# Optimization experiments

Measured on AMD Instinct MI355X. Metric: run time of the kernel, lower is better.

Reference implementation:

```python
import jax, jax.numpy as jnp
import numpy as np

EPS = float(np.finfo(np.float32).eps)
QMIN, QMAX = -128, 127


def setup_inputs() -> dict:
    key = jax.random.key(0)
    k_x, k_w, k_ws, k_b = jax.random.split(key, 4)
    M, K, N = 32768, 1024, 1024
    x = jax.random.normal(k_x, (M, K), dtype=jnp.float32)
    # per-channel symmetrically quantized, transposed weight: [K, N], values in [-128, 127]
    w_int8_t = jax.random.randint(k_w, (K, N), QMIN, QMAX + 1, dtype=jnp.int32).astype(jnp.int8)
    # per-out-channel scales (positive, float; torch uses float64, we use float32)
    w_scales = (jax.random.uniform(k_ws, (N,), dtype=jnp.float32) * 0.02 + 1e-4)
    # preprocessed column sums: w_int8_t.sum(dim=0)
    w_int8_t_sums = w_int8_t.astype(jnp.int32).sum(axis=0)
    bias = jax.random.normal(k_b, (N,), dtype=jnp.float32)
    return {
        "x": x,
        "w_int8_t": w_int8_t,
        "w_scales": w_scales,
        "w_int8_t_sums": w_int8_t_sums,
        "bias": bias,
    }


def reference(x, w_int8_t, w_scales, w_int8_t_sums, bias):
    # ---- dynamically_quantize_per_tensor (affine, int8) ----
    min_neg = jnp.minimum(jnp.min(x), jnp.float32(0.0))
    max_pos = jnp.maximum(jnp.max(x), jnp.float32(0.0))
    x_scale = jnp.maximum((max_pos - min_neg) / jnp.float32(QMAX - QMIN), EPS)
    x_zp = jnp.clip(QMIN - jnp.round(min_neg / x_scale), QMIN, QMAX)  # scalar
    x_q = jnp.clip(jnp.round(x / x_scale) + x_zp, QMIN, QMAX).astype(jnp.int8)

    # ---- int8 matmul with int32 accumulation (safe_int_mm equivalent) ----
    xw_i32 = jnp.matmul(
        x_q.astype(jnp.int32), w_int8_t.astype(jnp.int32)
    )  # [M, N] int32

    # ---- dequant with zero-point correction (quant_int8_matmul) ----
    mm_unscaled = xw_i32.astype(jnp.float32) - x_zp * w_int8_t_sums.astype(jnp.float32)
    y = x_scale * w_scales * mm_unscaled  # broadcast w_scales over N

    # ---- bias add (quant_int8_dynamic_linear) ----
    y = y + bias
    return y.astype(jnp.float32)
```

## Files before the change

kernel.cpp:

```cpp
#include <hip/hip_runtime.h>
#include <stdint.h>

#define M_DIM 32768
#define K_DIM 1024
#define N_DIM 1024

typedef int v4i __attribute__((ext_vector_type(4)));

__device__ __forceinline__ void gld_lds16(const void* g, void* lds) {
    __builtin_amdgcn_global_load_lds(
        (const __attribute__((address_space(1))) unsigned int*)g,
        (__attribute__((address_space(3))) unsigned int*)lds, 16, 0, 0);
}

__global__ void k_prep(const float* __restrict__ x,
                       float* __restrict__ pmin, float* __restrict__ pmax,
                       const int* __restrict__ w, int8_t* __restrict__ wt) {
    int t = threadIdx.x;
    if (blockIdx.x < 1024) {
        long gid = (long)blockIdx.x * 256 + t;
        const float4* x4 = (const float4*)x;
        const long n4 = (long)M_DIM * K_DIM / 4;
        float mn = INFINITY, mx = -INFINITY;
#pragma unroll 4
        for (long i = gid; i < n4; i += 1024 * 256) {
            float4 v = x4[i];
            mn = fminf(mn, fminf(fminf(v.x, v.y), fminf(v.z, v.w)));
            mx = fmaxf(mx, fmaxf(fmaxf(v.x, v.y), fmaxf(v.z, v.w)));
        }
        __shared__ float smn[256], smx[256];
        smn[t] = mn; smx[t] = mx;
        __syncthreads();
        for (int s = 128; s > 0; s >>= 1) {
            if (t < s) {
                smn[t] = fminf(smn[t], smn[t + s]);
                smx[t] = fmaxf(smx[t], smx[t + s]);
            }
            __syncthreads();
        }
        if (t == 0) { pmin[blockIdx.x] = smn[0]; pmax[blockIdx.x] = smx[0]; }
    } else {
        __shared__ int8_t tile[32][33];
        int b = blockIdx.x - 1024;
        int bn = (b & 31) * 32;
        int bk = (b >> 5) * 32;
        int tx = t & 31, ty = t >> 5;
#pragma unroll
        for (int i = 0; i < 32; i += 8)
            tile[ty + i][tx] = (int8_t)w[(long)(bk + ty + i) * N_DIM + bn + tx];
        __syncthreads();
#pragma unroll
        for (int i = 0; i < 32; i += 8)
            wt[(long)(bn + ty + i) * K_DIM + bk + tx] = tile[tx][ty + i];
    }
}

__device__ __forceinline__ unsigned q4(float4 v, float s, float zp) {
    int a = (int)fminf(fmaxf(rintf(v.x / s) + zp, -128.0f), 127.0f);
    int b = (int)fminf(fmaxf(rintf(v.y / s) + zp, -128.0f), 127.0f);
    int c = (int)fminf(fmaxf(rintf(v.z / s) + zp, -128.0f), 127.0f);
    int d = (int)fminf(fmaxf(rintf(v.w / s) + zp, -128.0f), 127.0f);
    return (a & 255) | ((b & 255) << 8) | ((c & 255) << 16) | ((d & 255) << 24);
}

__global__ void k_quant(const float* __restrict__ x,
                        const float* __restrict__ pmin,
                        const float* __restrict__ pmax,
                        float* __restrict__ sp,
                        int8_t* __restrict__ xq) {
    int t = threadIdx.x;
    float mn = INFINITY, mx = -INFINITY;
#pragma unroll
    for (int i = 0; i < 4; i++) {
        mn = fminf(mn, pmin[i * 256 + t]);
        mx = fmaxf(mx, pmax[i * 256 + t]);
    }
    __shared__ float smn[256], smx[256];
    smn[t] = mn; smx[t] = mx;
    __syncthreads();
    for (int ss = 128; ss > 0; ss >>= 1) {
        if (t < ss) {
            smn[t] = fminf(smn[t], smn[t + ss]);
            smx[t] = fmaxf(smx[t], smx[t + ss]);
        }
        __syncthreads();
    }
    float min_neg = fminf(smn[0], 0.0f);
    float max_pos = fmaxf(smx[0], 0.0f);
    float s = (max_pos - min_neg) / 255.0f;
    s = fmaxf(s, 1.1920928955078125e-07f);
    float zp = -128.0f - rintf(min_neg / s);
    zp = fminf(fmaxf(zp, -128.0f), 127.0f);
    if (blockIdx.x == 0 && t == 0) { sp[0] = s; sp[1] = zp; }

    const float4* x4 = (const float4*)x;
    unsigned* q4out = (unsigned*)xq;
    long base = (long)blockIdx.x * 1024;
#pragma unroll
    for (int v = 0; v < 4; v++) {
        long i = base + (long)v * 256 + t;
        float4 val = x4[i];
        q4out[i] = q4(val, s, zp);
    }
}

__global__ __launch_bounds__(256) void k_gemm(
    const int8_t* __restrict__ xq, const int8_t* __restrict__ wt,
    const float* __restrict__ sp, const float* __restrict__ w_scales,
    const int* __restrict__ wsums, const float* __restrict__ bias,
    float* __restrict__ out) {
    __shared__ __align__(16) int8_t lds_a[4][128 * 64];
    __shared__ __align__(16) int8_t lds_b[4][128 * 64];

    const int t = threadIdx.x;
    const int orig = blockIdx.x;
    const int swz = (orig & 7) * 256 + (orig >> 3);
    const int m0 = (swz >> 3) * 128;
    const int n0 = (swz & 7) * 128;
    const int w = t >> 6, l = t & 63, quad = l >> 4, r = l & 15;
    const int wave_m = (w & 1) * 64, wave_n = (w >> 1) * 64;

    v4i acc[4][4];
#pragma unroll
    for (int i = 0; i < 4; i++)
#pragma unroll
        for (int j = 0; j < 4; j++) acc[i][j] = (v4i){0, 0, 0, 0};

    const int slot0 = t, slot1 = 256 + t;
    const int row0 = slot0 >> 2, s0 = slot0 & 3;
    const int row1 = slot1 >> 2, s1 = slot1 & 3;
    const int q0 = s0 ^ (row0 & 3) ^ ((row0 >> 2) & 3);
    const int q1 = s1 ^ (row1 & 3) ^ ((row1 >> 2) & 3);
    const int8_t* gA0 = xq + (long)(m0 + row0) * K_DIM + q0 * 16;
    const int8_t* gA1 = xq + (long)(m0 + row1) * K_DIM + q1 * 16;
    const int8_t* gB0 = wt + (long)(n0 + row0) * K_DIM + q0 * 16;
    const int8_t* gB1 = wt + (long)(n0 + row1) * K_DIM + q1 * 16;

#define STAGE(buf, kb)                                        \
    do {                                                      \
        gld_lds16(gA0 + (kb), lds_a[buf] + slot0 * 16);       \
        gld_lds16(gA1 + (kb), lds_a[buf] + slot1 * 16);       \
        gld_lds16(gB0 + (kb), lds_b[buf] + slot0 * 16);       \
        gld_lds16(gB1 + (kb), lds_b[buf] + slot1 * 16);       \
    } while (0)

    int ra[4], rb[4];
#pragma unroll
    for (int i = 0; i < 4; i++) {
        int mrow = wave_m + i * 16 + r;
        int sa = quad ^ (mrow & 3) ^ ((mrow >> 2) & 3);
        ra[i] = mrow * 64 + sa * 16;
        int nrow = wave_n + i * 16 + r;
        int sb = quad ^ (nrow & 3) ^ ((nrow >> 2) & 3);
        rb[i] = nrow * 64 + sb * 16;
    }

    STAGE(0, 0);
    STAGE(1, 64);
    STAGE(2, 128);

#pragma unroll
    for (int kt = 0; kt < 16; ++kt) {
        if (kt <= 13)
            asm volatile("s_waitcnt vmcnt(8)" ::: "memory");
        else if (kt == 14)
            asm volatile("s_waitcnt vmcnt(4)" ::: "memory");
        else
            asm volatile("s_waitcnt vmcnt(0)" ::: "memory");
        asm volatile("s_barrier" ::: "memory");

        if (kt <= 12) STAGE((kt + 3) & 3, (kt + 3) * 64);

        v4i af[4], bf[4];
#pragma unroll
        for (int i = 0; i < 4; i++) af[i] = *(const v4i*)(lds_a[kt & 3] + ra[i]);
#pragma unroll
        for (int j = 0; j < 4; j++) bf[j] = *(const v4i*)(lds_b[kt & 3] + rb[j]);

        __builtin_amdgcn_s_setprio(1);
#pragma unroll
        for (int i = 0; i < 4; i++)
#pragma unroll
            for (int j = 0; j < 4; j++)
                acc[i][j] = __builtin_amdgcn_mfma_i32_16x16x64_i8(af[i], bf[j], acc[i][j], 0, 0, 0);
        __builtin_amdgcn_s_setprio(0);
    }
#undef STAGE

    const float scale = sp[0], zp = sp[1];
#pragma unroll
    for (int j = 0; j < 4; j++) {
        int n = n0 + wave_n + j * 16 + r;
        float sj = scale * w_scales[n];
        float cj = zp * (float)wsums[n];
        float bj = bias[n];
#pragma unroll
        for (int i = 0; i < 4; i++) {
            int mbase = m0 + wave_m + i * 16 + quad * 4;
#pragma unroll
            for (int e = 0; e < 4; e++) {
                out[(long)(mbase + e) * N_DIM + n] = sj * ((float)acc[i][j][e] - cj) + bj;
            }
        }
    }
}

extern "C" void kernel_launch(void* const* d_in, const int* in_sizes, int n_in,
                              void* d_out, int out_size, void* d_ws, size_t ws_size,
                              hipStream_t stream) {
    const float* x        = (const float*)d_in[0];
    const int*   w_int8_t = (const int*)d_in[1];
    const float* w_scales = (const float*)d_in[2];
    const int*   w_sums   = (const int*)d_in[3];
    const float* bias     = (const float*)d_in[4];
    float* out = (float*)d_out;

    float* wsf  = (float*)d_ws;
    float* pmin = wsf;
    float* pmax = wsf + 1024;
    float* sp   = wsf + 2048;
    int8_t* wt  = (int8_t*)d_ws + 16384;
    int8_t* xq  = (int8_t*)d_ws + 16384 + (size_t)K_DIM * N_DIM;

    k_prep<<<2048, 256, 0, stream>>>(x, pmin, pmax, w_int8_t, wt);
    k_quant<<<8192, 256, 0, stream>>>(x, pmin, pmax, sp, xq);
    k_gemm<<<2048, 256, 0, stream>>>(xq, wt, sp, w_scales, w_sums, bias, out);
}
```

Measured before the change: 305.4 us.

## Fuse activation quantization into GEMM with full-K LDS A tile and register-streamed B

Removes the separate quantization kernel and its int8 intermediate buffer. Each 512-thread block now quantizes a 64-row strip of x straight into a 64KB swizzled LDS tile covering all of K. Its eight waves each compute 128 output columns, streaming weights from global memory into double-buffered registers instead of staging them through LDS. This saves the xq write/read round trip and a kernel launch. In exchange, weight traffic rises because every block rereads the whole weight matrix, there are only 512 blocks, and register pressure is high (32 accumulators plus 16 B vectors).

```diff
diff --git a/kernel.cpp b/kernel.cpp
--- a/kernel.cpp
+++ b/kernel.cpp
@@ -6,12 +6,6 @@
 #define N_DIM 1024
 
 typedef int v4i __attribute__((ext_vector_type(4)));
-
-__device__ __forceinline__ void gld_lds16(const void* g, void* lds) {
-    __builtin_amdgcn_global_load_lds(
-        (const __attribute__((address_space(1))) unsigned int*)g,
-        (__attribute__((address_space(3))) unsigned int*)lds, 16, 0, 0);
-}
 
 __global__ void k_prep(const float* __restrict__ x,
                        float* __restrict__ pmin, float* __restrict__ pmax,
@@ -63,143 +57,107 @@
     return (a & 255) | ((b & 255) << 8) | ((c & 255) << 16) | ((d & 255) << 24);
 }
 
-__global__ void k_quant(const float* __restrict__ x,
-                        const float* __restrict__ pmin,
-                        const float* __restrict__ pmax,
-                        float* __restrict__ sp,
-                        int8_t* __restrict__ xq) {
-    int t = threadIdx.x;
-    float mn = INFINITY, mx = -INFINITY;
-#pragma unroll
-    for (int i = 0; i < 4; i++) {
-        mn = fminf(mn, pmin[i * 256 + t]);
-        mx = fmaxf(mx, pmax[i * 256 + t]);
-    }
-    __shared__ float smn[256], smx[256];
-    smn[t] = mn; smx[t] = mx;
+__global__ __launch_bounds__(512, 2) void k_gemm(
+    const float* __restrict__ x, const int8_t* __restrict__ wt,
+    const float* __restrict__ pmin, const float* __restrict__ pmax,
+    const float* __restrict__ w_scales, const int* __restrict__ wsums,
+    const float* __restrict__ bias, float* __restrict__ out) {
+    __shared__ __align__(16) int8_t lds_a[64 * 1024];
+    __shared__ float red[2][512];
+
+    const int t = threadIdx.x;
+    const int m0 = blockIdx.x * 64;
+
+    red[0][t] = fminf(pmin[t], pmin[t + 512]);
+    red[1][t] = fmaxf(pmax[t], pmax[t + 512]);
     __syncthreads();
-    for (int ss = 128; ss > 0; ss >>= 1) {
+    for (int ss = 256; ss > 0; ss >>= 1) {
         if (t < ss) {
-            smn[t] = fminf(smn[t], smn[t + ss]);
-            smx[t] = fmaxf(smx[t], smx[t + ss]);
+            red[0][t] = fminf(red[0][t], red[0][t + ss]);
+            red[1][t] = fmaxf(red[1][t], red[1][t + ss]);
         }
         __syncthreads();
     }
-    float min_neg = fminf(smn[0], 0.0f);
-    float max_pos = fmaxf(smx[0], 0.0f);
+    const float min_neg = fminf(red[0][0], 0.0f);
+    const float max_pos = fmaxf(red[1][0], 0.0f);
     float s = (max_pos - min_neg) / 255.0f;
     s = fmaxf(s, 1.1920928955078125e-07f);
     float zp = -128.0f - rintf(min_neg / s);
     zp = fminf(fmaxf(zp, -128.0f), 127.0f);
-    if (blockIdx.x == 0 && t == 0) { sp[0] = s; sp[1] = zp; }
 
-    const float4* x4 = (const float4*)x;
-    unsigned* q4out = (unsigned*)xq;
-    long base = (long)blockIdx.x * 1024;
+    {
+        const float4* xp = (const float4*)(x + (long)m0 * K_DIM);
 #pragma unroll
-    for (int v = 0; v < 4; v++) {
-        long i = base + (long)v * 256 + t;
-        float4 val = x4[i];
-        q4out[i] = q4(val, s, zp);
+        for (int v = 0; v < 32; v++) {
+            int i = v * 512 + t;
+            int row = i >> 8, f4 = i & 255;
+            float4 val = xp[i];
+            unsigned u = q4(val, s, zp);
+            int quad = f4 >> 2;
+            int slot = quad ^ (row & 7);
+            *(unsigned*)(lds_a + row * 1024 + slot * 16 + (f4 & 3) * 4) = u;
+        }
     }
-}
+    __syncthreads();
 
-__global__ __launch_bounds__(256) void k_gemm(
-    const int8_t* __restrict__ xq, const int8_t* __restrict__ wt,
-    const float* __restrict__ sp, const float* __restrict__ w_scales,
-    const int* __restrict__ wsums, const float* __restrict__ bias,
-    float* __restrict__ out) {
-    __shared__ __align__(16) int8_t lds_a[4][128 * 64];
-    __shared__ __align__(16) int8_t lds_b[4][128 * 64];
+    const int wv = t >> 6, l = t & 63, quad = l >> 4, r = l & 15;
+    const int n0w = wv * 128;
 
-    const int t = threadIdx.x;
-    const int orig = blockIdx.x;
-    const int swz = (orig & 7) * 256 + (orig >> 3);
-    const int m0 = (swz >> 3) * 128;
-    const int n0 = (swz & 7) * 128;
-    const int w = t >> 6, l = t & 63, quad = l >> 4, r = l & 15;
-    const int wave_m = (w & 1) * 64, wave_n = (w >> 1) * 64;
+    int mbase[4], xm[4];
+#pragma unroll
+    for (int i = 0; i < 4; i++) {
+        int m = i * 16 + r;
+        mbase[i] = m * 1024;
+        xm[i] = m & 7;
+    }
+    const int8_t* bp = wt + (long)(n0w + r) * K_DIM + quad * 16;
 
-    v4i acc[4][4];
+    v4i acc[4][8];
 #pragma unroll
     for (int i = 0; i < 4; i++)
 #pragma unroll
-        for (int j = 0; j < 4; j++) acc[i][j] = (v4i){0, 0, 0, 0};
+        for (int j = 0; j < 8; j++) acc[i][j] = (v4i){0, 0, 0, 0};
 
-    const int slot0 = t, slot1 = 256 + t;
-    const int row0 = slot0 >> 2, s0 = slot0 & 3;
-    const int row1 = slot1 >> 2, s1 = slot1 & 3;
-    const int q0 = s0 ^ (row0 & 3) ^ ((row0 >> 2) & 3);
-    const int q1 = s1 ^ (row1 & 3) ^ ((row1 >> 2) & 3);
-    const int8_t* gA0 = xq + (long)(m0 + row0) * K_DIM + q0 * 16;
-    const int8_t* gA1 = xq + (long)(m0 + row1) * K_DIM + q1 * 16;
-    const int8_t* gB0 = wt + (long)(n0 + row0) * K_DIM + q0 * 16;
-    const int8_t* gB1 = wt + (long)(n0 + row1) * K_DIM + q1 * 16;
-
-#define STAGE(buf, kb)                                        \
-    do {                                                      \
-        gld_lds16(gA0 + (kb), lds_a[buf] + slot0 * 16);       \
-        gld_lds16(gA1 + (kb), lds_a[buf] + slot1 * 16);       \
-        gld_lds16(gB0 + (kb), lds_b[buf] + slot0 * 16);       \
-        gld_lds16(gB1 + (kb), lds_b[buf] + slot1 * 16);       \
-    } while (0)
-
-    int ra[4], rb[4];
+    v4i breg[2][8];
 #pragma unroll
-    for (int i = 0; i < 4; i++) {
-        int mrow = wave_m + i * 16 + r;
-        int sa = quad ^ (mrow & 3) ^ ((mrow >> 2) & 3);
-        ra[i] = mrow * 64 + sa * 16;
-        int nrow = wave_n + i * 16 + r;
-        int sb = quad ^ (nrow & 3) ^ ((nrow >> 2) & 3);
-        rb[i] = nrow * 64 + sb * 16;
-    }
-
-    STAGE(0, 0);
-    STAGE(1, 64);
-    STAGE(2, 128);
+    for (int j = 0; j < 8; j++)
+        breg[0][j] = *(const v4i*)(bp + j * 16 * K_DIM);
 
 #pragma unroll
-    for (int kt = 0; kt < 16; ++kt) {
-        if (kt <= 13)
-            asm volatile("s_waitcnt vmcnt(8)" ::: "memory");
-        else if (kt == 14)
-            asm volatile("s_waitcnt vmcnt(4)" ::: "memory");
-        else
-            asm volatile("s_waitcnt vmcnt(0)" ::: "memory");
-        asm volatile("s_barrier" ::: "memory");
-
-        if (kt <= 12) STAGE((kt + 3) & 3, (kt + 3) * 64);
-
-        v4i af[4], bf[4];
+    for (int kt = 0; kt < 16; kt++) {
+        if (kt < 15) {
 #pragma unroll
-        for (int i = 0; i < 4; i++) af[i] = *(const v4i*)(lds_a[kt & 3] + ra[i]);
+            for (int j = 0; j < 8; j++)
+                breg[(kt + 1) & 1][j] = *(const v4i*)(bp + j * 16 * K_DIM + (kt + 1) * 64);
+        }
+        v4i af[4];
 #pragma unroll
-        for (int j = 0; j < 4; j++) bf[j] = *(const v4i*)(lds_b[kt & 3] + rb[j]);
-
+        for (int i = 0; i < 4; i++) {
+            int slot = (kt * 4 + quad) ^ xm[i];
+            af[i] = *(const v4i*)(lds_a + mbase[i] + slot * 16);
+        }
         __builtin_amdgcn_s_setprio(1);
 #pragma unroll
         for (int i = 0; i < 4; i++)
 #pragma unroll
-            for (int j = 0; j < 4; j++)
-                acc[i][j] = __builtin_amdgcn_mfma_i32_16x16x64_i8(af[i], bf[j], acc[i][j], 0, 0, 0);
+            for (int j = 0; j < 8; j++)
+                acc[i][j] = __builtin_amdgcn_mfma_i32_16x16x64_i8(
+                    af[i], breg[kt & 1][j], acc[i][j], 0, 0, 0);
         __builtin_amdgcn_s_setprio(0);
     }
-#undef STAGE
 
-    const float scale = sp[0], zp = sp[1];
 #pragma unroll
-    for (int j = 0; j < 4; j++) {
-        int n = n0 + wave_n + j * 16 + r;
-        float sj = scale * w_scales[n];
+    for (int j = 0; j < 8; j++) {
+        int n = n0w + j * 16 + r;
+        float sj = s * w_scales[n];
         float cj = zp * (float)wsums[n];
         float bj = bias[n];
 #pragma unroll
         for (int i = 0; i < 4; i++) {
-            int mbase = m0 + wave_m + i * 16 + quad * 4;
+            int mrow = m0 + i * 16 + quad * 4;
 #pragma unroll
             for (int e = 0; e < 4; e++) {
-                out[(long)(mbase + e) * N_DIM + n] = sj * ((float)acc[i][j][e] - cj) + bj;
+                out[(long)(mrow + e) * N_DIM + n] = sj * ((float)acc[i][j][e] - cj) + bj;
             }
         }
     }
@@ -218,11 +176,8 @@
     float* wsf  = (float*)d_ws;
     float* pmin = wsf;
     float* pmax = wsf + 1024;
-    float* sp   = wsf + 2048;
     int8_t* wt  = (int8_t*)d_ws + 16384;
-    int8_t* xq  = (int8_t*)d_ws + 16384 + (size_t)K_DIM * N_DIM;
 
     k_prep<<<2048, 256, 0, stream>>>(x, pmin, pmax, w_int8_t, wt);
-    k_quant<<<8192, 256, 0, stream>>>(x, pmin, pmax, sp, xq);
-    k_gemm<<<2048, 256, 0, stream>>>(xq, wt, sp, w_scales, w_sums, bias, out);
+    k_gemm<<<512, 512, 0, stream>>>(x, wt, pmin, pmax, w_scales, w_sums, bias, out);
 }
```

Measured after the change: 324.8 us. 6.3% more time.
